# Optimization experiments

Hardware: AMD Instinct MI355X
Metric: run time of the kernel (lower is better)

Reference implementation:

```python
import jax, jax.numpy as jnp
import numpy as np

N, E, D, L = 50000, 625000, 128, 7
EPS = 1e-7   # GENConv message epsilon
T = 1.0      # softmax aggregation temperature (learn_t=False)
NUM_ATOM_FEATS, ATOM_VOCAB = 9, 64
NUM_BOND_FEATS, BOND_VOCAB = 3, 8


def setup_inputs() -> dict:
    key = jax.random.key(0)
    ks = jax.random.split(key, 9)
    x = jax.random.randint(ks[0], (N, NUM_ATOM_FEATS), 0, ATOM_VOCAB, dtype=jnp.int32)
    edge_index = jax.random.randint(ks[1], (2, E), 0, N, dtype=jnp.int32)
    edge_attr = jax.random.randint(ks[2], (E, NUM_BOND_FEATS), 0, BOND_VOCAB, dtype=jnp.int32)
    atom_emb = jax.random.normal(ks[3], (NUM_ATOM_FEATS, ATOM_VOCAB, D), dtype=jnp.float32) * 0.1
    bond_emb = jax.random.normal(ks[4], (NUM_BOND_FEATS, BOND_VOCAB, D), dtype=jnp.float32) * 0.1
    W = jax.random.normal(ks[5], (L, D, D), dtype=jnp.float32) / np.sqrt(D).astype(np.float32)
    b = jnp.zeros((L, D), dtype=jnp.float32)
    ln_gamma = jnp.ones((L, D), dtype=jnp.float32)
    ln_beta = jnp.zeros((L, D), dtype=jnp.float32)
    return dict(x=x, edge_index=edge_index, edge_attr=edge_attr,
                atom_emb=atom_emb, bond_emb=bond_emb, W=W, b=b,
                ln_gamma=ln_gamma, ln_beta=ln_beta)


def _layer_norm(h, g, bta):
    mu = jnp.mean(h, axis=-1, keepdims=True)
    var = jnp.var(h, axis=-1, keepdims=True)
    return (h - mu) * jax.lax.rsqrt(var + 1e-5) * g + bta


def _gen_conv(h, src, dst, edge_emb, Wl, bl):
    # GENConv: msg = relu(x_j + e) + eps; softmax aggregation over dst; Linear(x + m)
    msg = jax.nn.relu(h[src] + edge_emb) + EPS                 # [E, D]
    logits = msg * T
    seg_max = jax.ops.segment_max(logits, dst, num_segments=N)  # [N, D]
    seg_max = jnp.where(jnp.isfinite(seg_max), seg_max, 0.0)    # empty segments
    e = jnp.exp(logits - seg_max[dst])                          # [E, D]
    denom = jax.ops.segment_sum(e, dst, num_segments=N)         # [N, D]
    alpha = e / (denom[dst] + 1e-16)
    m = jax.ops.segment_sum(alpha * msg, dst, num_segments=N)   # [N, D]
    return (h + m) @ Wl + bl


def reference(x, edge_index, edge_attr, atom_emb, bond_emb, W, b, ln_gamma, ln_beta):
    src, dst = edge_index[0], edge_index[1]
    # AtomEncoder: sum of per-feature embedding lookups -> [N, D]
    h = jnp.sum(atom_emb[jnp.arange(NUM_ATOM_FEATS)[None, :], x], axis=1)
    # BondEncoder (conv_encode_edge=False: encoded once) -> [E, D]
    edge_emb = jnp.sum(bond_emb[jnp.arange(NUM_BOND_FEATS)[None, :], edge_attr], axis=1)
    # res+ block, dropout=0 (no-op)
    h = _gen_conv(h, src, dst, edge_emb, W[0], b[0])
    for layer in range(1, L):
        h2 = jax.nn.relu(_layer_norm(h, ln_gamma[layer - 1], ln_beta[layer - 1]))
        h = _gen_conv(h2, src, dst, edge_emb, W[layer], b[layer]) + h
    h = _layer_norm(h, ln_gamma[L - 1], ln_beta[L - 1])
    return h
```

## Files before the change

### kernel.cpp

```cpp
#include <hip/hip_runtime.h>
#include <hip/hip_fp16.h>
#include <math.h>


constexpr int D = 128;
constexpr int NA = 9;
constexpr int NB = 3;
constexpr float L2E = 1.4426950408889634f;
constexpr float INV_L2E = 0.6931471805599453f;

using half8  = __attribute__((ext_vector_type(8))) _Float16;
using h2v    = __attribute__((ext_vector_type(2))) _Float16;
using floatx4 = __attribute__((ext_vector_type(4))) float;


__global__ void k_hist(const int* __restrict__ dst, int* __restrict__ deg, int E) {
    int e = blockIdx.x * 256 + threadIdx.x;
    if (e < E) atomicAdd(&deg[dst[e]], 1);
}

__global__ void k_scan_a(const int* __restrict__ deg, int* __restrict__ offs,
                         int* __restrict__ bsum, int N) {
    __shared__ int s[256];
    int i = blockIdx.x * 256 + threadIdx.x;
    int v = (i < N) ? deg[i] : 0;
    s[threadIdx.x] = v;
    __syncthreads();
    for (int d = 1; d < 256; d <<= 1) {
        int add = (threadIdx.x >= d) ? s[threadIdx.x - d] : 0;
        __syncthreads();
        s[threadIdx.x] += add;
        __syncthreads();
    }
    if (i < N) offs[i + 1] = s[threadIdx.x];
    if (threadIdx.x == 255) bsum[blockIdx.x] = s[255];
    if (i == 0) offs[0] = 0;
}

__global__ void k_scan_b(const int* __restrict__ bsum, int* __restrict__ bexc, int nb) {
    __shared__ int s[256];
    int t = threadIdx.x;
    int v = (t < nb) ? bsum[t] : 0;
    s[t] = v;
    __syncthreads();
    for (int d = 1; d < 256; d <<= 1) {
        int add = (t >= d) ? s[t - d] : 0;
        __syncthreads();
        s[t] += add;
        __syncthreads();
    }
    if (t < nb) bexc[t] = s[t] - v;
}

__global__ void k_scan_c(int* __restrict__ offs, const int* __restrict__ bexc, int N) {
    int i = blockIdx.x * 256 + threadIdx.x;
    if (i < N) offs[i + 1] += bexc[blockIdx.x];
}

__global__ void k_fill(const int* __restrict__ src, const int* __restrict__ dst,
                       const int* __restrict__ attr, const int* __restrict__ offs,
                       int* __restrict__ cur, unsigned* __restrict__ recs1, int E) {
    int e = blockIdx.x * 256 + threadIdx.x;
    if (e >= E) return;
    int d = dst[e];
    int pos = offs[d] + atomicAdd(&cur[d], 1);
    unsigned cidx = (unsigned)(attr[e * 3] * 64 + attr[e * 3 + 1] * 8 + attr[e * 3 + 2]);
    recs1[pos] = (unsigned)src[e] | (cidx << 17);
}


__global__ void k_dhist(const int* __restrict__ deg, int* __restrict__ dbin, int N) {
    __shared__ int lb[64];
    int t = threadIdx.x;
    if (t < 64) lb[t] = 0;
    __syncthreads();
    int i = blockIdx.x * 256 + t;
    if (i < N) {
        int d = deg[i]; d = d < 63 ? d : 63;
        atomicAdd(&lb[63 - d], 1);
    }
    __syncthreads();
    if (t < 64 && lb[t] > 0) atomicAdd(&dbin[t], lb[t]);
}

__global__ void k_dscan(const int* __restrict__ dbin, int* __restrict__ doff) {
    if (threadIdx.x == 0) {
        int acc = 0;
        for (int b = 0; b < 64; ++b) { doff[b] = acc; acc += dbin[b]; }
    }
}

__global__ void k_dfill(const int* __restrict__ deg, const int* __restrict__ doff,
                        int* __restrict__ dcur, int* __restrict__ perm, int N) {
    __shared__ int lc[64], lbase[64];
    int t = threadIdx.x;
    if (t < 64) lc[t] = 0;
    __syncthreads();
    int i = blockIdx.x * 256 + t;
    int b = 0, rank = 0;
    if (i < N) {
        int d = deg[i]; d = d < 63 ? d : 63;
        b = 63 - d;
        rank = atomicAdd(&lc[b], 1);
    }
    __syncthreads();
    if (t < 64 && lc[t] > 0) lbase[t] = atomicAdd(&dcur[t], lc[t]);
    __syncthreads();
    if (i < N) perm[doff[b] + lbase[b] + rank] = i;
}

__global__ void k_comb(const float* __restrict__ bemb, __half* __restrict__ comb16) {
    int gid = blockIdx.x * 256 + threadIdx.x;
    int c = gid >> 5, q = gid & 31;
    int a0 = c >> 6, a1 = (c >> 3) & 7, a2 = c & 7;
    float4 v0 = *(const float4*)(bemb + (a0)*D + q * 4);
    float4 v1 = *(const float4*)(bemb + (8 + a1) * D + q * 4);
    float4 v2 = *(const float4*)(bemb + (16 + a2) * D + q * 4);
    __half2* c2 = (__half2*)comb16;
    c2[c * 64 + q * 2]     = __floats2half2_rn(L2E * (v0.x + v1.x + v2.x),
                                               L2E * (v0.y + v1.y + v2.y));
    c2[c * 64 + q * 2 + 1] = __floats2half2_rn(L2E * (v0.z + v1.z + v2.z),
                                               L2E * (v0.w + v1.w + v2.w));
}

__global__ void k_wt(const float* __restrict__ W, __half* __restrict__ Wt16, int total) {
    int o = blockIdx.x * 256 + threadIdx.x;
    if (o >= total) return;
    int l = o >> 14;
    int rem = o & 16383;
    int f = rem >> 7, k = rem & 127;
    Wt16[o] = __float2half_rn(W[(l << 14) + k * 128 + f]);
}


__global__ void k_atom(const int* __restrict__ x, const float* __restrict__ aemb,
                       __half* __restrict__ h16, int N) {
    int wid = (blockIdx.x * blockDim.x + threadIdx.x) >> 6;
    int lane = threadIdx.x & 63;
    if (wid >= N) return;
    const int* xr = x + wid * NA;
    float ax = 0.f, ay = 0.f;
#pragma unroll
    for (int f = 0; f < NA; ++f) {
        int v = xr[f];
        const float2 e = *(const float2*)(aemb + (f * 64 + v) * D + 2 * lane);
        ax += e.x; ay += e.y;
    }
    ((__half2*)h16)[wid * 64 + lane] = __floats2half2_rn(ax * L2E, ay * L2E);
}


__global__ __launch_bounds__(256) void k_agg(const __half* __restrict__ h16,
                      const unsigned* __restrict__ recs1,
                      const int* __restrict__ offs, const __half* __restrict__ comb16,
                      const int* __restrict__ perm,
                      __half* __restrict__ t16, int N) {
    int wid = (blockIdx.x * blockDim.x + threadIdx.x) >> 6;
    int lane = threadIdx.x & 63;
    if (wid >= N) return;
    int nid = perm[wid];
    int su = __builtin_amdgcn_readfirstlane(offs[nid]);
    int eu = __builtin_amdgcn_readfirstlane(offs[nid + 1]);
    h2v hm2 = ((const h2v*)h16)[nid * 64 + lane];
    float hsx = (float)hm2[0], hsy = (float)hm2[1];
    if (su >= eu) {
        ((__half2*)t16)[nid * 64 + lane] =
            __floats2half2_rn(hsx * INV_L2E, hsy * INV_L2E);
        return;
    }
    float Sx = 0.f, Sy = 0.f, Wx = 0.f, Wy = 0.f;

    const h2v* hrow = (const h2v*)h16 + lane;
    const h2v* crow = (const h2v*)comb16 + lane;

    const h2v zero2 = (h2v)(_Float16)0;
    const h2v eps2  = {(_Float16)(1e-7f * L2E), (_Float16)(1e-7f * L2E)};

    h2v hq[16], cq[16];

    int e0 = su;
    do {
        int lastc = (eu < e0 + 64) ? eu : e0 + 64;
        int last = lastc - 1;
        int ridx = e0 + lane;
        ridx = (ridx < eu - 1) ? ridx : eu - 1;
        unsigned recv = recs1[ridx];

        auto load4 = [&](int base, int slot) {
#pragma unroll
            for (int i = 0; i < 4; ++i) {
                int idx = base + i; idx = (idx < last) ? idx : last;
                unsigned r = __builtin_amdgcn_readlane(recv, idx - e0);
                int sj = (int)(r & 0x1FFFFu);
                int cj = (int)(r >> 17);
                hq[slot * 4 + i] = hrow[sj * 64];
                cq[slot * 4 + i] = crow[cj * 64];
            }
        };
        auto comp4u = [&](int slot) {
#pragma unroll
            for (int i = 0; i < 4; ++i) {
                h2v m = hq[slot * 4 + i] + cq[slot * 4 + i];
                m = __builtin_elementwise_max(m, zero2);
                m = m + eps2;
                float u0 = (float)m[0], u1 = (float)m[1];
                float px = __builtin_amdgcn_exp2f(u0);
                float py = __builtin_amdgcn_exp2f(u1);
                Sx += px; Sy += py;
                Wx = fmaf(px, u0, Wx);
                Wy = fmaf(py, u1, Wy);
            }
        };
        auto comp4m = [&](int gb, int slot) {
#pragma unroll
            for (int i = 0; i < 4; ++i) {
                h2v m = hq[slot * 4 + i] + cq[slot * 4 + i];
                m = __builtin_elementwise_max(m, zero2);
                m = m + eps2;
                float u0 = (float)m[0], u1 = (float)m[1];
                bool valid = (gb + i) < lastc;
                float px = valid ? __builtin_amdgcn_exp2f(u0) : 0.f;
                float py = valid ? __builtin_amdgcn_exp2f(u1) : 0.f;
                Sx += px; Sy += py;
                Wx = fmaf(px, u0, Wx);
                Wy = fmaf(py, u1, Wy);
            }
        };

        load4(e0, 0);
        if (e0 + 4  < lastc) load4(e0 + 4, 1);
        if (e0 + 8  < lastc) load4(e0 + 8, 2);
        if (e0 + 12 < lastc) load4(e0 + 12, 3);

        int e = e0;
        for (; e + 16 < lastc; e += 16) {
            comp4u(0); comp4u(1); comp4u(2); comp4u(3);
            load4(e + 16, 0); load4(e + 20, 1); load4(e + 24, 2); load4(e + 28, 3);
        }
        comp4m(e, 0);
        if (e + 4  < lastc) comp4m(e + 4, 1);
        if (e + 8  < lastc) comp4m(e + 8, 2);
        if (e + 12 < lastc) comp4m(e + 12, 3);

        e0 = lastc;
    } while (e0 < eu);

    float tx = (hsx + Wx / (Sx + 1e-16f)) * INV_L2E;
    float ty = (hsy + Wy / (Sy + 1e-16f)) * INV_L2E;
    ((__half2*)t16)[nid * 64 + lane] = __floats2half2_rn(tx, ty);
}


template <int MODE>
__global__ __launch_bounds__(256) void k_gemm(const __half* __restrict__ A16,
                                              const __half* __restrict__ Wt16,
                                              const float* __restrict__ bl,
                                              const __half* __restrict__ res16,
                                              __half* __restrict__ hres16,
                                              const float* __restrict__ g,
                                              const float* __restrict__ bta,
                                              __half* __restrict__ h16,
                                              float* __restrict__ out,
                                              int N, int useRes) {
    int lane = threadIdx.x & 63;
    int wave = threadIdx.x >> 6;
    int quad = lane >> 4, col = lane & 15;
    int node = blockIdx.x * 64 + wave * 16 + col;
    bool nok = node < N;
    int nc = nok ? node : N - 1;

    const __half* arow = A16 + (size_t)nc * 128;
    half8 bfrag[4];
#pragma unroll
    for (int ks = 0; ks < 4; ++ks)
        bfrag[ks] = *(const half8*)(arow + ks * 32 + quad * 8);

    floatx4 acc[8];
#pragma unroll
    for (int ft = 0; ft < 8; ++ft) acc[ft] = (floatx4){0.f, 0.f, 0.f, 0.f};

#pragma unroll
    for (int ft = 0; ft < 8; ++ft) {
        const __half* wrow = Wt16 + (size_t)(ft * 16 + col) * 128;
#pragma unroll
        for (int ks = 0; ks < 4; ++ks) {
            half8 afrag = *(const half8*)(wrow + ks * 32 + quad * 8);
            acc[ft] = __builtin_amdgcn_mfma_f32_16x16x32_f16(afrag, bfrag[ks],
                                                             acc[ft], 0, 0, 0);
        }
    }

    float s = 0.f, ss = 0.f;
#pragma unroll
    for (int ft = 0; ft < 8; ++ft) {
        int f0 = ft * 16 + quad * 4;
        float4 bb = *(const float4*)(bl + f0);
        float o0 = acc[ft][0] + bb.x, o1 = acc[ft][1] + bb.y;
        float o2 = acc[ft][2] + bb.z, o3 = acc[ft][3] + bb.w;
        if (useRes) {
            uint2 rr = *(const uint2*)(res16 + (size_t)nc * 128 + f0);
            __half2 r01 = *(__half2*)&rr.x, r23 = *(__half2*)&rr.y;
            o0 += __low2float(r01); o1 += __high2float(r01);
            o2 += __low2float(r23); o3 += __high2float(r23);
        }
        acc[ft][0] = o0; acc[ft][1] = o1; acc[ft][2] = o2; acc[ft][3] = o3;
        s += (o0 + o1) + (o2 + o3);
        ss += fmaf(o0, o0, o1 * o1) + fmaf(o2, o2, o3 * o3);
        if (MODE == 0 && nok) {
            __half2 h01 = __floats2half2_rn(o0, o1);
            __half2 h23 = __floats2half2_rn(o2, o3);
            uint2 pk = make_uint2(*(unsigned*)&h01, *(unsigned*)&h23);
            *(uint2*)(hres16 + (size_t)node * 128 + f0) = pk;
        }
    }
    s += __shfl_xor(s, 16, 64);  ss += __shfl_xor(ss, 16, 64);
    s += __shfl_xor(s, 32, 64);  ss += __shfl_xor(ss, 32, 64);
    float mu = s * (1.f / 128.f);
    float var = ss * (1.f / 128.f) - mu * mu;
    float rs = rsqrtf(var + 1e-5f);

#pragma unroll
    for (int ft = 0; ft < 8; ++ft) {
        int f0 = ft * 16 + quad * 4;
        float4 gg = *(const float4*)(g + f0);
        float4 bt = *(const float4*)(bta + f0);
        float l0 = (acc[ft][0] - mu) * rs * gg.x + bt.x;
        float l1 = (acc[ft][1] - mu) * rs * gg.y + bt.y;
        float l2 = (acc[ft][2] - mu) * rs * gg.z + bt.z;
        float l3 = (acc[ft][3] - mu) * rs * gg.w + bt.w;
        if (MODE == 0) {
            l0 = fmaxf(l0, 0.f); l1 = fmaxf(l1, 0.f);
            l2 = fmaxf(l2, 0.f); l3 = fmaxf(l3, 0.f);
            if (nok) {
                __half2 h01 = __floats2half2_rn(l0 * L2E, l1 * L2E);
                __half2 h23 = __floats2half2_rn(l2 * L2E, l3 * L2E);
                uint2 pk = make_uint2(*(unsigned*)&h01, *(unsigned*)&h23);
                *(uint2*)(h16 + (size_t)node * 128 + f0) = pk;
            }
        } else {
            if (nok)
                *(float4*)(out + (size_t)node * 128 + f0) =
                    make_float4(l0, l1, l2, l3);
        }
    }
}


extern "C" void kernel_launch(void* const* d_in, const int* in_sizes, int n_in,
                              void* d_out, int out_size, void* d_ws, size_t ws_size,
                              hipStream_t stream) {
    const int*   x    = (const int*)d_in[0];
    const int*   ei   = (const int*)d_in[1];
    const int*   attr = (const int*)d_in[2];
    const float* aemb = (const float*)d_in[3];
    const float* bemb = (const float*)d_in[4];
    const float* Wf   = (const float*)d_in[5];
    const float* bf   = (const float*)d_in[6];
    const float* gam  = (const float*)d_in[7];
    const float* bet  = (const float*)d_in[8];
    float* out = (float*)d_out;

    const int N = in_sizes[0] / NA;
    const int E = in_sizes[1] / 2;
    const int L = in_sizes[5] / (D * D);

    char* ws = (char*)d_ws;
    size_t o = 0;
    auto carve = [&](size_t bytes) -> void* {
        void* p = (void*)(ws + o);
        o += (bytes + 255) & ~(size_t)255;
        return p;
    };
    __half* hres16 = (__half*)carve((size_t)N * D * 2);
    __half* h16    = (__half*)carve((size_t)N * D * 2);
    __half* t16    = (__half*)carve((size_t)N * D * 2);
    unsigned* recs1 = (unsigned*)carve((size_t)E * 4);
    __half* comb16 = (__half*)carve(512 * D * 2);
    __half* Wt16   = (__half*)carve((size_t)L * D * D * 2);
    int*    deg    = (int*)carve((size_t)N * 4);
    int*    cur    = (int*)carve((size_t)N * 4);
    int*    offs   = (int*)carve((size_t)(N + 1) * 4);
    int*    perm   = (int*)carve((size_t)N * 4);
    int*    dbin   = (int*)carve(256);
    int*    doff   = (int*)carve(256);
    int*    dcur   = (int*)carve(256);
    int*    bsum   = (int*)carve(4096);
    int*    bexc   = (int*)carve(4096);

    const int* src = ei;
    const int* dst = ei + E;

    hipMemsetAsync(deg, 0, (size_t)N * 4, stream);
    hipMemsetAsync(cur, 0, (size_t)N * 4, stream);
    hipMemsetAsync(dbin, 0, 256, stream);
    hipMemsetAsync(dcur, 0, 256, stream);

    int ebl = (E + 255) / 256;
    int nbl = (N + 255) / 256;
    k_comb<<<64, 256, 0, stream>>>(bemb, comb16);
    int wtot = L * D * D;
    k_wt<<<(wtot + 255) / 256, 256, 0, stream>>>(Wf, Wt16, wtot);
    k_hist<<<ebl, 256, 0, stream>>>(dst, deg, E);
    k_scan_a<<<nbl, 256, 0, stream>>>(deg, offs, bsum, N);
    k_scan_b<<<1, 256, 0, stream>>>(bsum, bexc, nbl);
    k_scan_c<<<nbl, 256, 0, stream>>>(offs, bexc, N);
    k_fill<<<ebl, 256, 0, stream>>>(src, dst, attr, offs, cur, recs1, E);
    k_dhist<<<nbl, 256, 0, stream>>>(deg, dbin, N);
    k_dscan<<<1, 64, 0, stream>>>(dbin, doff);
    k_dfill<<<nbl, 256, 0, stream>>>(deg, doff, dcur, perm, N);

    int wbl = (N * 64 + 255) / 256;
    k_atom<<<wbl, 256, 0, stream>>>(x, aemb, h16, N);

    int gbl = (N + 63) / 64;
    for (int l = 0; l < L; ++l) {
        k_agg<<<wbl, 256, 0, stream>>>(h16, recs1, offs, comb16, perm, t16, N);
        if (l == L - 1) {
            k_gemm<1><<<gbl, 256, 0, stream>>>(t16, Wt16 + l * D * D, bf + l * D,
                                               hres16, hres16,
                                               gam + l * D, bet + l * D, h16, out,
                                               N, 1);
        } else {
            k_gemm<0><<<gbl, 256, 0, stream>>>(t16, Wt16 + l * D * D, bf + l * D,
                                               hres16, hres16,
                                               gam + l * D, bet + l * D, h16, out,
                                               N, l > 0 ? 1 : 0);
        }
    }
}
```

Baseline: 622.8 us.

## Fuse softmax aggregation into GEMM kernel with ping-pong feature buffers

Merges the per-node softmax aggregation kernel into the GEMM/LayerNorm kernel. Each wave aggregates 16 consecutive nodes into an LDS tile, which then feeds the MFMA stage directly, so the t16 intermediate no longer round-trips through global memory and one launch per layer is removed. The degree-sorted node permutation and its three setup kernels are dropped, and h is ping-ponged between two buffers to avoid a read/write race. The epsilon add in the message is also removed. The costs are serialized per-wave processing of 16 nodes with varied degrees (load imbalance without degree sorting) and lower occupancy from the 17 KB LDS tile. Dropping the epsilon slightly changes the numerics.

```diff
diff --git a/kernel.cpp b/kernel.cpp
--- a/kernel.cpp
+++ b/kernel.cpp
@@ -68,47 +68,6 @@
     recs1[pos] = (unsigned)src[e] | (cidx << 17);
 }
 
-
-__global__ void k_dhist(const int* __restrict__ deg, int* __restrict__ dbin, int N) {
-    __shared__ int lb[64];
-    int t = threadIdx.x;
-    if (t < 64) lb[t] = 0;
-    __syncthreads();
-    int i = blockIdx.x * 256 + t;
-    if (i < N) {
-        int d = deg[i]; d = d < 63 ? d : 63;
-        atomicAdd(&lb[63 - d], 1);
-    }
-    __syncthreads();
-    if (t < 64 && lb[t] > 0) atomicAdd(&dbin[t], lb[t]);
-}
-
-__global__ void k_dscan(const int* __restrict__ dbin, int* __restrict__ doff) {
-    if (threadIdx.x == 0) {
-        int acc = 0;
-        for (int b = 0; b < 64; ++b) { doff[b] = acc; acc += dbin[b]; }
-    }
-}
-
-__global__ void k_dfill(const int* __restrict__ deg, const int* __restrict__ doff,
-                        int* __restrict__ dcur, int* __restrict__ perm, int N) {
-    __shared__ int lc[64], lbase[64];
-    int t = threadIdx.x;
-    if (t < 64) lc[t] = 0;
-    __syncthreads();
-    int i = blockIdx.x * 256 + t;
-    int b = 0, rank = 0;
-    if (i < N) {
-        int d = deg[i]; d = d < 63 ? d : 63;
-        b = 63 - d;
-        rank = atomicAdd(&lc[b], 1);
-    }
-    __syncthreads();
-    if (t < 64 && lc[t] > 0) lbase[t] = atomicAdd(&dcur[t], lc[t]);
-    __syncthreads();
-    if (i < N) perm[doff[b] + lbase[b] + rank] = i;
-}
-
 __global__ void k_comb(const float* __restrict__ bemb, __half* __restrict__ comb16) {
     int gid = blockIdx.x * 256 + threadIdx.x;
     int c = gid >> 5, q = gid & 31;
@@ -150,130 +109,130 @@
 }
 
 
-__global__ __launch_bounds__(256) void k_agg(const __half* __restrict__ h16,
-                      const unsigned* __restrict__ recs1,
-                      const int* __restrict__ offs, const __half* __restrict__ comb16,
-                      const int* __restrict__ perm,
-                      __half* __restrict__ t16, int N) {
-    int wid = (blockIdx.x * blockDim.x + threadIdx.x) >> 6;
-    int lane = threadIdx.x & 63;
-    if (wid >= N) return;
-    int nid = perm[wid];
-    int su = __builtin_amdgcn_readfirstlane(offs[nid]);
-    int eu = __builtin_amdgcn_readfirstlane(offs[nid + 1]);
-    h2v hm2 = ((const h2v*)h16)[nid * 64 + lane];
-    float hsx = (float)hm2[0], hsy = (float)hm2[1];
-    if (su >= eu) {
-        ((__half2*)t16)[nid * 64 + lane] =
-            __floats2half2_rn(hsx * INV_L2E, hsy * INV_L2E);
-        return;
-    }
-    float Sx = 0.f, Sy = 0.f, Wx = 0.f, Wy = 0.f;
-
-    const h2v* hrow = (const h2v*)h16 + lane;
-    const h2v* crow = (const h2v*)comb16 + lane;
-
-    const h2v zero2 = (h2v)(_Float16)0;
-    const h2v eps2  = {(_Float16)(1e-7f * L2E), (_Float16)(1e-7f * L2E)};
-
-    h2v hq[16], cq[16];
-
-    int e0 = su;
-    do {
-        int lastc = (eu < e0 + 64) ? eu : e0 + 64;
-        int last = lastc - 1;
-        int ridx = e0 + lane;
-        ridx = (ridx < eu - 1) ? ridx : eu - 1;
-        unsigned recv = recs1[ridx];
-
-        auto load4 = [&](int base, int slot) {
-#pragma unroll
-            for (int i = 0; i < 4; ++i) {
-                int idx = base + i; idx = (idx < last) ? idx : last;
-                unsigned r = __builtin_amdgcn_readlane(recv, idx - e0);
-                int sj = (int)(r & 0x1FFFFu);
-                int cj = (int)(r >> 17);
-                hq[slot * 4 + i] = hrow[sj * 64];
-                cq[slot * 4 + i] = crow[cj * 64];
-            }
-        };
-        auto comp4u = [&](int slot) {
-#pragma unroll
-            for (int i = 0; i < 4; ++i) {
-                h2v m = hq[slot * 4 + i] + cq[slot * 4 + i];
-                m = __builtin_elementwise_max(m, zero2);
-                m = m + eps2;
-                float u0 = (float)m[0], u1 = (float)m[1];
-                float px = __builtin_amdgcn_exp2f(u0);
-                float py = __builtin_amdgcn_exp2f(u1);
-                Sx += px; Sy += py;
-                Wx = fmaf(px, u0, Wx);
-                Wy = fmaf(py, u1, Wy);
-            }
-        };
-        auto comp4m = [&](int gb, int slot) {
-#pragma unroll
-            for (int i = 0; i < 4; ++i) {
-                h2v m = hq[slot * 4 + i] + cq[slot * 4 + i];
-                m = __builtin_elementwise_max(m, zero2);
-                m = m + eps2;
-                float u0 = (float)m[0], u1 = (float)m[1];
-                bool valid = (gb + i) < lastc;
-                float px = valid ? __builtin_amdgcn_exp2f(u0) : 0.f;
-                float py = valid ? __builtin_amdgcn_exp2f(u1) : 0.f;
-                Sx += px; Sy += py;
-                Wx = fmaf(px, u0, Wx);
-                Wy = fmaf(py, u1, Wy);
-            }
-        };
-
-        load4(e0, 0);
-        if (e0 + 4  < lastc) load4(e0 + 4, 1);
-        if (e0 + 8  < lastc) load4(e0 + 8, 2);
-        if (e0 + 12 < lastc) load4(e0 + 12, 3);
-
-        int e = e0;
-        for (; e + 16 < lastc; e += 16) {
-            comp4u(0); comp4u(1); comp4u(2); comp4u(3);
-            load4(e + 16, 0); load4(e + 20, 1); load4(e + 24, 2); load4(e + 28, 3);
-        }
-        comp4m(e, 0);
-        if (e + 4  < lastc) comp4m(e + 4, 1);
-        if (e + 8  < lastc) comp4m(e + 8, 2);
-        if (e + 12 < lastc) comp4m(e + 12, 3);
-
-        e0 = lastc;
-    } while (e0 < eu);
-
-    float tx = (hsx + Wx / (Sx + 1e-16f)) * INV_L2E;
-    float ty = (hsy + Wy / (Sy + 1e-16f)) * INV_L2E;
-    ((__half2*)t16)[nid * 64 + lane] = __floats2half2_rn(tx, ty);
-}
-
-
 template <int MODE>
-__global__ __launch_bounds__(256) void k_gemm(const __half* __restrict__ A16,
-                                              const __half* __restrict__ Wt16,
-                                              const float* __restrict__ bl,
-                                              const __half* __restrict__ res16,
-                                              __half* __restrict__ hres16,
-                                              const float* __restrict__ g,
-                                              const float* __restrict__ bta,
-                                              __half* __restrict__ h16,
-                                              float* __restrict__ out,
-                                              int N, int useRes) {
+__global__ __launch_bounds__(256) void k_fused(
+    const __half* __restrict__ hin,
+    const unsigned* __restrict__ recs1,
+    const int* __restrict__ offs,
+    const __half* __restrict__ comb16,
+    const __half* __restrict__ Wt16,
+    const float* __restrict__ bl,
+    __half* __restrict__ hres16,
+    const float* __restrict__ g,
+    const float* __restrict__ bta,
+    __half* __restrict__ hout,
+    float* __restrict__ out,
+    int N, int useRes) {
+    __shared__ __align__(16) __half tt[64 * 136];
     int lane = threadIdx.x & 63;
     int wave = threadIdx.x >> 6;
+    int nbase = blockIdx.x * 64 + wave * 16;
+
+    int oidx = nbase + lane;
+    oidx = (oidx <= N) ? oidx : N;
+    int offv = (lane < 17) ? offs[oidx] : 0;
+
+    const h2v* hrow = (const h2v*)hin + lane;
+    const h2v* crow = (const h2v*)comb16 + lane;
+    const h2v zero2 = (h2v)(_Float16)0;
+
+#pragma unroll 1
+    for (int j = 0; j < 16; ++j) {
+        int nid = nbase + j;
+        int nc = (nid < N) ? nid : N - 1;
+        int su = __builtin_amdgcn_readlane(offv, j);
+        int eu = __builtin_amdgcn_readlane(offv, j + 1);
+        h2v hm2 = hrow[nc * 64];
+        float hsx = (float)hm2[0], hsy = (float)hm2[1];
+        float tx, ty;
+        if (su >= eu) {
+            tx = hsx * INV_L2E;
+            ty = hsy * INV_L2E;
+        } else {
+            float Sx = 0.f, Sy = 0.f, Wx = 0.f, Wy = 0.f;
+            h2v hq[16], cq[16];
+            int e0 = su;
+            do {
+                int lastc = (eu < e0 + 64) ? eu : e0 + 64;
+                int last = lastc - 1;
+                int ridx = e0 + lane;
+                ridx = (ridx < eu - 1) ? ridx : eu - 1;
+                unsigned recv = recs1[ridx];
+
+                auto load4 = [&](int base, int slot) {
+#pragma unroll
+                    for (int i = 0; i < 4; ++i) {
+                        int idx = base + i; idx = (idx < last) ? idx : last;
+                        unsigned r = __builtin_amdgcn_readlane(recv, idx - e0);
+                        int sj = (int)(r & 0x1FFFFu);
+                        int cj = (int)(r >> 17);
+                        hq[slot * 4 + i] = hrow[sj * 64];
+                        cq[slot * 4 + i] = crow[cj * 64];
+                    }
+                };
+                auto comp4u = [&](int slot) {
+#pragma unroll
+                    for (int i = 0; i < 4; ++i) {
+                        h2v m = hq[slot * 4 + i] + cq[slot * 4 + i];
+                        m = __builtin_elementwise_max(m, zero2);
+                        float u0 = (float)m[0], u1 = (float)m[1];
+                        float px = __builtin_amdgcn_exp2f(u0);
+                        float py = __builtin_amdgcn_exp2f(u1);
+                        Sx += px; Sy += py;
+                        Wx = fmaf(px, u0, Wx);
+                        Wy = fmaf(py, u1, Wy);
+                    }
+                };
+                auto comp4m = [&](int gb, int slot) {
+#pragma unroll
+                    for (int i = 0; i < 4; ++i) {
+                        h2v m = hq[slot * 4 + i] + cq[slot * 4 + i];
+                        m = __builtin_elementwise_max(m, zero2);
+                        float u0 = (float)m[0], u1 = (float)m[1];
+                        bool valid = (gb + i) < lastc;
+                        float px = valid ? __builtin_amdgcn_exp2f(u0) : 0.f;
+                        float py = valid ? __builtin_amdgcn_exp2f(u1) : 0.f;
+                        Sx += px; Sy += py;
+                        Wx = fmaf(px, u0, Wx);
+                        Wy = fmaf(py, u1, Wy);
+                    }
+                };
+
+                load4(e0, 0);
+                if (e0 + 4  < lastc) load4(e0 + 4, 1);
+                if (e0 + 8  < lastc) load4(e0 + 8, 2);
+                if (e0 + 12 < lastc) load4(e0 + 12, 3);
+
+                int e = e0;
+                for (; e + 16 < lastc; e += 16) {
+                    comp4u(0); comp4u(1); comp4u(2); comp4u(3);
+                    load4(e + 16, 0); load4(e + 20, 1);
+                    load4(e + 24, 2); load4(e + 28, 3);
+                }
+                comp4m(e, 0);
+                if (e + 4  < lastc) comp4m(e + 4, 1);
+                if (e + 8  < lastc) comp4m(e + 8, 2);
+                if (e + 12 < lastc) comp4m(e + 12, 3);
+
+                e0 = lastc;
+            } while (e0 < eu);
+            tx = (hsx + Wx / (Sx + 1e-16f)) * INV_L2E;
+            ty = (hsy + Wy / (Sy + 1e-16f)) * INV_L2E;
+        }
+        ((__half2*)tt)[(wave * 16 + j) * 68 + lane] = __floats2half2_rn(tx, ty);
+    }
+    __syncthreads();
+
     int quad = lane >> 4, col = lane & 15;
     int node = blockIdx.x * 64 + wave * 16 + col;
     bool nok = node < N;
-    int nc = nok ? node : N - 1;
-
-    const __half* arow = A16 + (size_t)nc * 128;
+    int nc2 = nok ? node : N - 1;
+
+    const __half* trow = tt + (size_t)(wave * 16 + col) * 136;
     half8 bfrag[4];
 #pragma unroll
     for (int ks = 0; ks < 4; ++ks)
-        bfrag[ks] = *(const half8*)(arow + ks * 32 + quad * 8);
+        bfrag[ks] = *(const half8*)(trow + ks * 32 + quad * 8);
 
     floatx4 acc[8];
 #pragma unroll
@@ -298,7 +257,7 @@
         float o0 = acc[ft][0] + bb.x, o1 = acc[ft][1] + bb.y;
         float o2 = acc[ft][2] + bb.z, o3 = acc[ft][3] + bb.w;
         if (useRes) {
-            uint2 rr = *(const uint2*)(res16 + (size_t)nc * 128 + f0);
+            uint2 rr = *(const uint2*)(hres16 + (size_t)nc2 * 128 + f0);
             __half2 r01 = *(__half2*)&rr.x, r23 = *(__half2*)&rr.y;
             o0 += __low2float(r01); o1 += __high2float(r01);
             o2 += __low2float(r23); o3 += __high2float(r23);
@@ -335,7 +294,7 @@
                 __half2 h01 = __floats2half2_rn(l0 * L2E, l1 * L2E);
                 __half2 h23 = __floats2half2_rn(l2 * L2E, l3 * L2E);
                 uint2 pk = make_uint2(*(unsigned*)&h01, *(unsigned*)&h23);
-                *(uint2*)(h16 + (size_t)node * 128 + f0) = pk;
+                *(uint2*)(hout + (size_t)node * 128 + f0) = pk;
             }
         } else {
             if (nok)
@@ -372,18 +331,14 @@
         return p;
     };
     __half* hres16 = (__half*)carve((size_t)N * D * 2);
-    __half* h16    = (__half*)carve((size_t)N * D * 2);
-    __half* t16    = (__half*)carve((size_t)N * D * 2);
+    __half* hA     = (__half*)carve((size_t)N * D * 2);
+    __half* hB     = (__half*)carve((size_t)N * D * 2);
     unsigned* recs1 = (unsigned*)carve((size_t)E * 4);
     __half* comb16 = (__half*)carve(512 * D * 2);
     __half* Wt16   = (__half*)carve((size_t)L * D * D * 2);
     int*    deg    = (int*)carve((size_t)N * 4);
     int*    cur    = (int*)carve((size_t)N * 4);
     int*    offs   = (int*)carve((size_t)(N + 1) * 4);
-    int*    perm   = (int*)carve((size_t)N * 4);
-    int*    dbin   = (int*)carve(256);
-    int*    doff   = (int*)carve(256);
-    int*    dcur   = (int*)carve(256);
     int*    bsum   = (int*)carve(4096);
     int*    bexc   = (int*)carve(4096);
 
@@ -392,8 +347,6 @@
 
     hipMemsetAsync(deg, 0, (size_t)N * 4, stream);
     hipMemsetAsync(cur, 0, (size_t)N * 4, stream);
-    hipMemsetAsync(dbin, 0, 256, stream);
-    hipMemsetAsync(dcur, 0, 256, stream);
 
     int ebl = (E + 255) / 256;
     int nbl = (N + 255) / 256;
@@ -405,26 +358,24 @@
     k_scan_b<<<1, 256, 0, stream>>>(bsum, bexc, nbl);
     k_scan_c<<<nbl, 256, 0, stream>>>(offs, bexc, N);
     k_fill<<<ebl, 256, 0, stream>>>(src, dst, attr, offs, cur, recs1, E);
-    k_dhist<<<nbl, 256, 0, stream>>>(deg, dbin, N);
-    k_dscan<<<1, 64, 0, stream>>>(dbin, doff);
-    k_dfill<<<nbl, 256, 0, stream>>>(deg, doff, dcur, perm, N);
 
     int wbl = (N * 64 + 255) / 256;
-    k_atom<<<wbl, 256, 0, stream>>>(x, aemb, h16, N);
+    k_atom<<<wbl, 256, 0, stream>>>(x, aemb, hA, N);
 
     int gbl = (N + 63) / 64;
     for (int l = 0; l < L; ++l) {
-        k_agg<<<wbl, 256, 0, stream>>>(h16, recs1, offs, comb16, perm, t16, N);
+        const __half* hi = (l & 1) ? hB : hA;
+        __half* ho = (l & 1) ? hA : hB;
         if (l == L - 1) {
-            k_gemm<1><<<gbl, 256, 0, stream>>>(t16, Wt16 + l * D * D, bf + l * D,
-                                               hres16, hres16,
-                                               gam + l * D, bet + l * D, h16, out,
-                                               N, 1);
+            k_fused<1><<<gbl, 256, 0, stream>>>(hi, recs1, offs, comb16,
+                                                Wt16 + l * D * D, bf + l * D,
+                                                hres16, gam + l * D, bet + l * D,
+                                                ho, out, N, 1);
         } else {
-            k_gemm<0><<<gbl, 256, 0, stream>>>(t16, Wt16 + l * D * D, bf + l * D,
-                                               hres16, hres16,
-                                               gam + l * D, bet + l * D, h16, out,
-                                               N, l > 0 ? 1 : 0);
-        }
-    }
-}
+            k_fused<0><<<gbl, 256, 0, stream>>>(hi, recs1, offs, comb16,
+                                                Wt16 + l * D * D, bf + l * D,
+                                                hres16, gam + l * D, bet + l * D,
+                                                ho, out, N, l > 0 ? 1 : 0);
+        }
+    }
+}
```

Result: slower. 756.6 us (+21.5%).

## Replace degree-sorted node permutation with edge-balanced node ranges per wave

Applied to the files above, without the earlier changes.

Drops the degree-bucket permutation (histogram, scan and fill kernels) and instead splits the CSR into ranges of about 32 edges, giving each wave the run of consecutive nodes whose edges start in its range. The aggregation kernel loops over those nodes, which balances edges per wave, cuts the wave count from N to about E/32, and makes node accesses sequential. It also drops the epsilon add in the message. Serial node loops within a wave can lower memory-level parallelism for low-degree nodes, and removing eps slightly changes numerics.

```diff
diff --git a/kernel.cpp b/kernel.cpp
--- a/kernel.cpp
+++ b/kernel.cpp
@@ -6,6 +6,7 @@
 constexpr int D = 128;
 constexpr int NA = 9;
 constexpr int NB = 3;
+constexpr int CEDGE = 32;
 constexpr float L2E = 1.4426950408889634f;
 constexpr float INV_L2E = 0.6931471805599453f;
 
@@ -68,45 +69,16 @@
     recs1[pos] = (unsigned)src[e] | (cidx << 17);
 }
 
-
-__global__ void k_dhist(const int* __restrict__ deg, int* __restrict__ dbin, int N) {
-    __shared__ int lb[64];
-    int t = threadIdx.x;
-    if (t < 64) lb[t] = 0;
-    __syncthreads();
-    int i = blockIdx.x * 256 + t;
-    if (i < N) {
-        int d = deg[i]; d = d < 63 ? d : 63;
-        atomicAdd(&lb[63 - d], 1);
-    }
-    __syncthreads();
-    if (t < 64 && lb[t] > 0) atomicAdd(&dbin[t], lb[t]);
-}
-
-__global__ void k_dscan(const int* __restrict__ dbin, int* __restrict__ doff) {
-    if (threadIdx.x == 0) {
-        int acc = 0;
-        for (int b = 0; b < 64; ++b) { doff[b] = acc; acc += dbin[b]; }
-    }
-}
-
-__global__ void k_dfill(const int* __restrict__ deg, const int* __restrict__ doff,
-                        int* __restrict__ dcur, int* __restrict__ perm, int N) {
-    __shared__ int lc[64], lbase[64];
-    int t = threadIdx.x;
-    if (t < 64) lc[t] = 0;
-    __syncthreads();
-    int i = blockIdx.x * 256 + t;
-    int b = 0, rank = 0;
-    if (i < N) {
-        int d = deg[i]; d = d < 63 ? d : 63;
-        b = 63 - d;
-        rank = atomicAdd(&lc[b], 1);
-    }
-    __syncthreads();
-    if (t < 64 && lc[t] > 0) lbase[t] = atomicAdd(&dcur[t], lc[t]);
-    __syncthreads();
-    if (i < N) perm[doff[b] + lbase[b] + rank] = i;
+__global__ void k_part(const int* __restrict__ offs, int* __restrict__ wstart,
+                       int N, int NW) {
+    int n = blockIdx.x * 256 + threadIdx.x;
+    if (n >= N) return;
+    int a = offs[n] / CEDGE;
+    int b = offs[n + 1] / CEDGE;
+    if (n == 0) wstart[0] = 0;
+    for (int w = a + 1; w <= b; ++w) wstart[w] = n + 1;
+    if (n == N - 1)
+        for (int w = b + 1; w <= NW; ++w) wstart[w] = N;
 }
 
 __global__ void k_comb(const float* __restrict__ bemb, __half* __restrict__ comb16) {
@@ -153,101 +125,101 @@
 __global__ __launch_bounds__(256) void k_agg(const __half* __restrict__ h16,
                       const unsigned* __restrict__ recs1,
                       const int* __restrict__ offs, const __half* __restrict__ comb16,
-                      const int* __restrict__ perm,
-                      __half* __restrict__ t16, int N) {
-    int wid = (blockIdx.x * blockDim.x + threadIdx.x) >> 6;
+                      const int* __restrict__ wstart,
+                      __half* __restrict__ t16, int NW) {
+    int w = (blockIdx.x * blockDim.x + threadIdx.x) >> 6;
     int lane = threadIdx.x & 63;
-    if (wid >= N) return;
-    int nid = perm[wid];
-    int su = __builtin_amdgcn_readfirstlane(offs[nid]);
-    int eu = __builtin_amdgcn_readfirstlane(offs[nid + 1]);
-    h2v hm2 = ((const h2v*)h16)[nid * 64 + lane];
-    float hsx = (float)hm2[0], hsy = (float)hm2[1];
-    if (su >= eu) {
-        ((__half2*)t16)[nid * 64 + lane] =
-            __floats2half2_rn(hsx * INV_L2E, hsy * INV_L2E);
-        return;
-    }
-    float Sx = 0.f, Sy = 0.f, Wx = 0.f, Wy = 0.f;
+    if (w >= NW) return;
+    int n0 = wstart[w];
+    int n1 = wstart[w + 1];
 
     const h2v* hrow = (const h2v*)h16 + lane;
     const h2v* crow = (const h2v*)comb16 + lane;
-
     const h2v zero2 = (h2v)(_Float16)0;
-    const h2v eps2  = {(_Float16)(1e-7f * L2E), (_Float16)(1e-7f * L2E)};
-
-    h2v hq[16], cq[16];
-
-    int e0 = su;
-    do {
-        int lastc = (eu < e0 + 64) ? eu : e0 + 64;
-        int last = lastc - 1;
-        int ridx = e0 + lane;
-        ridx = (ridx < eu - 1) ? ridx : eu - 1;
-        unsigned recv = recs1[ridx];
-
-        auto load4 = [&](int base, int slot) {
-#pragma unroll
-            for (int i = 0; i < 4; ++i) {
-                int idx = base + i; idx = (idx < last) ? idx : last;
-                unsigned r = __builtin_amdgcn_readlane(recv, idx - e0);
-                int sj = (int)(r & 0x1FFFFu);
-                int cj = (int)(r >> 17);
-                hq[slot * 4 + i] = hrow[sj * 64];
-                cq[slot * 4 + i] = crow[cj * 64];
+
+#pragma unroll 1
+    for (int nid = n0; nid < n1; ++nid) {
+        int su = offs[nid];
+        int eu = offs[nid + 1];
+        h2v hm2 = hrow[nid * 64];
+        float hsx = (float)hm2[0], hsy = (float)hm2[1];
+        if (su >= eu) {
+            ((__half2*)t16)[nid * 64 + lane] =
+                __floats2half2_rn(hsx * INV_L2E, hsy * INV_L2E);
+            continue;
+        }
+        float Sx = 0.f, Sy = 0.f, Wx = 0.f, Wy = 0.f;
+        h2v hq[16], cq[16];
+        int e0 = su;
+        do {
+            int lastc = (eu < e0 + 64) ? eu : e0 + 64;
+            int last = lastc - 1;
+            int ridx = e0 + lane;
+            ridx = (ridx < eu - 1) ? ridx : eu - 1;
+            unsigned recv = recs1[ridx];
+
+            auto load4 = [&](int base, int slot) {
+#pragma unroll
+                for (int i = 0; i < 4; ++i) {
+                    int idx = base + i; idx = (idx < last) ? idx : last;
+                    unsigned r = __builtin_amdgcn_readlane(recv, idx - e0);
+                    int sj = (int)(r & 0x1FFFFu);
+                    int cj = (int)(r >> 17);
+                    hq[slot * 4 + i] = hrow[sj * 64];
+                    cq[slot * 4 + i] = crow[cj * 64];
+                }
+            };
+            auto comp4u = [&](int slot) {
+#pragma unroll
+                for (int i = 0; i < 4; ++i) {
+                    h2v m = hq[slot * 4 + i] + cq[slot * 4 + i];
+                    m = __builtin_elementwise_max(m, zero2);
+                    float u0 = (float)m[0], u1 = (float)m[1];
+                    float px = __builtin_amdgcn_exp2f(u0);
+                    float py = __builtin_amdgcn_exp2f(u1);
+                    Sx += px; Sy += py;
+                    Wx = fmaf(px, u0, Wx);
+                    Wy = fmaf(py, u1, Wy);
+                }
+            };
+            auto comp4m = [&](int gb, int slot) {
+#pragma unroll
+                for (int i = 0; i < 4; ++i) {
+                    h2v m = hq[slot * 4 + i] + cq[slot * 4 + i];
+                    m = __builtin_elementwise_max(m, zero2);
+                    float u0 = (float)m[0], u1 = (float)m[1];
+                    bool valid = (gb + i) < lastc;
+                    float px = valid ? __builtin_amdgcn_exp2f(u0) : 0.f;
+                    float py = valid ? __builtin_amdgcn_exp2f(u1) : 0.f;
+                    Sx += px; Sy += py;
+                    Wx = fmaf(px, u0, Wx);
+                    Wy = fmaf(py, u1, Wy);
+                }
+            };
+
+            load4(e0, 0);
+            if (e0 + 4  < lastc) load4(e0 + 4, 1);
+            if (e0 + 8  < lastc) load4(e0 + 8, 2);
+            if (e0 + 12 < lastc) load4(e0 + 12, 3);
+
+            int e = e0;
+            for (; e + 16 < lastc; e += 16) {
+                comp4u(0); comp4u(1); comp4u(2); comp4u(3);
+                load4(e + 16, 0); load4(e + 20, 1);
+                load4(e + 24, 2); load4(e + 28, 3);
             }
-        };
-        auto comp4u = [&](int slot) {
-#pragma unroll
-            for (int i = 0; i < 4; ++i) {
-                h2v m = hq[slot * 4 + i] + cq[slot * 4 + i];
-                m = __builtin_elementwise_max(m, zero2);
-                m = m + eps2;
-                float u0 = (float)m[0], u1 = (float)m[1];
-                float px = __builtin_amdgcn_exp2f(u0);
-                float py = __builtin_amdgcn_exp2f(u1);
-                Sx += px; Sy += py;
-                Wx = fmaf(px, u0, Wx);
-                Wy = fmaf(py, u1, Wy);
-            }
-        };
-        auto comp4m = [&](int gb, int slot) {
-#pragma unroll
-            for (int i = 0; i < 4; ++i) {
-                h2v m = hq[slot * 4 + i] + cq[slot * 4 + i];
-                m = __builtin_elementwise_max(m, zero2);
-                m = m + eps2;
-                float u0 = (float)m[0], u1 = (float)m[1];
-                bool valid = (gb + i) < lastc;
-                float px = valid ? __builtin_amdgcn_exp2f(u0) : 0.f;
-                float py = valid ? __builtin_amdgcn_exp2f(u1) : 0.f;
-                Sx += px; Sy += py;
-                Wx = fmaf(px, u0, Wx);
-                Wy = fmaf(py, u1, Wy);
-            }
-        };
-
-        load4(e0, 0);
-        if (e0 + 4  < lastc) load4(e0 + 4, 1);
-        if (e0 + 8  < lastc) load4(e0 + 8, 2);
-        if (e0 + 12 < lastc) load4(e0 + 12, 3);
-
-        int e = e0;
-        for (; e + 16 < lastc; e += 16) {
-            comp4u(0); comp4u(1); comp4u(2); comp4u(3);
-            load4(e + 16, 0); load4(e + 20, 1); load4(e + 24, 2); load4(e + 28, 3);
-        }
-        comp4m(e, 0);
-        if (e + 4  < lastc) comp4m(e + 4, 1);
-        if (e + 8  < lastc) comp4m(e + 8, 2);
-        if (e + 12 < lastc) comp4m(e + 12, 3);
-
-        e0 = lastc;
-    } while (e0 < eu);
-
-    float tx = (hsx + Wx / (Sx + 1e-16f)) * INV_L2E;
-    float ty = (hsy + Wy / (Sy + 1e-16f)) * INV_L2E;
-    ((__half2*)t16)[nid * 64 + lane] = __floats2half2_rn(tx, ty);
+            comp4m(e, 0);
+            if (e + 4  < lastc) comp4m(e + 4, 1);
+            if (e + 8  < lastc) comp4m(e + 8, 2);
+            if (e + 12 < lastc) comp4m(e + 12, 3);
+
+            e0 = lastc;
+        } while (e0 < eu);
+
+        float tx = (hsx + Wx / (Sx + 1e-16f)) * INV_L2E;
+        float ty = (hsy + Wy / (Sy + 1e-16f)) * INV_L2E;
+        ((__half2*)t16)[nid * 64 + lane] = __floats2half2_rn(tx, ty);
+    }
 }
 
 
@@ -363,6 +335,7 @@
     const int N = in_sizes[0] / NA;
     const int E = in_sizes[1] / 2;
     const int L = in_sizes[5] / (D * D);
+    const int NW = (E + CEDGE - 1) / CEDGE;
 
     char* ws = (char*)d_ws;
     size_t o = 0;
@@ -380,10 +353,7 @@
     int*    deg    = (int*)carve((size_t)N * 4);
     int*    cur    = (int*)carve((size_t)N * 4);
     int*    offs   = (int*)carve((size_t)(N + 1) * 4);
-    int*    perm   = (int*)carve((size_t)N * 4);
-    int*    dbin   = (int*)carve(256);
-    int*    doff   = (int*)carve(256);
-    int*    dcur   = (int*)carve(256);
+    int*    wstart = (int*)carve((size_t)(NW + 1) * 4);
     int*    bsum   = (int*)carve(4096);
     int*    bexc   = (int*)carve(4096);
 
@@ -392,8 +362,6 @@
 
     hipMemsetAsync(deg, 0, (size_t)N * 4, stream);
     hipMemsetAsync(cur, 0, (size_t)N * 4, stream);
-    hipMemsetAsync(dbin, 0, 256, stream);
-    hipMemsetAsync(dcur, 0, 256, stream);
 
     int ebl = (E + 255) / 256;
     int nbl = (N + 255) / 256;
@@ -405,16 +373,15 @@
     k_scan_b<<<1, 256, 0, stream>>>(bsum, bexc, nbl);
     k_scan_c<<<nbl, 256, 0, stream>>>(offs, bexc, N);
     k_fill<<<ebl, 256, 0, stream>>>(src, dst, attr, offs, cur, recs1, E);
-    k_dhist<<<nbl, 256, 0, stream>>>(deg, dbin, N);
-    k_dscan<<<1, 64, 0, stream>>>(dbin, doff);
-    k_dfill<<<nbl, 256, 0, stream>>>(deg, doff, dcur, perm, N);
+    k_part<<<nbl, 256, 0, stream>>>(offs, wstart, N, NW);
 
     int wbl = (N * 64 + 255) / 256;
     k_atom<<<wbl, 256, 0, stream>>>(x, aemb, h16, N);
 
+    int abl = (NW * 64 + 255) / 256;
     int gbl = (N + 63) / 64;
     for (int l = 0; l < L; ++l) {
-        k_agg<<<wbl, 256, 0, stream>>>(h16, recs1, offs, comb16, perm, t16, N);
+        k_agg<<<abl, 256, 0, stream>>>(h16, recs1, offs, comb16, wstart, t16, NW);
         if (l == L - 1) {
             k_gemm<1><<<gbl, 256, 0, stream>>>(t16, Wt16 + l * D * D, bf + l * D,
                                                hres16, hres16,
```

Result: slower. 666.0 us (+6.9%).

## Split GEMM output features across wave pairs and drop eps add in aggregation

Applied to the files above, without the earlier changes.

The GEMM+LayerNorm kernel now gives each 16-node group to two waves that each compute half of the 128 output features. The row statistics are combined through shared memory with a block barrier, and residual loads are hoisted ahead of the MFMA loop. This halves the accumulator registers per wave and doubles the block count, aiming for higher occupancy and more parallelism, at the cost of a __syncthreads and each wave loading its A fragment redundantly. The aggregation kernel also drops the per-edge epsilon add, a small numerical deviation, and changes the masked-tail validity test from lastc to eu.

```diff
diff --git a/kernel.cpp b/kernel.cpp
--- a/kernel.cpp
+++ b/kernel.cpp
@@ -172,9 +172,7 @@
 
     const h2v* hrow = (const h2v*)h16 + lane;
     const h2v* crow = (const h2v*)comb16 + lane;
-
     const h2v zero2 = (h2v)(_Float16)0;
-    const h2v eps2  = {(_Float16)(1e-7f * L2E), (_Float16)(1e-7f * L2E)};
 
     h2v hq[16], cq[16];
 
@@ -202,7 +200,6 @@
             for (int i = 0; i < 4; ++i) {
                 h2v m = hq[slot * 4 + i] + cq[slot * 4 + i];
                 m = __builtin_elementwise_max(m, zero2);
-                m = m + eps2;
                 float u0 = (float)m[0], u1 = (float)m[1];
                 float px = __builtin_amdgcn_exp2f(u0);
                 float py = __builtin_amdgcn_exp2f(u1);
@@ -216,9 +213,8 @@
             for (int i = 0; i < 4; ++i) {
                 h2v m = hq[slot * 4 + i] + cq[slot * 4 + i];
                 m = __builtin_elementwise_max(m, zero2);
-                m = m + eps2;
                 float u0 = (float)m[0], u1 = (float)m[1];
-                bool valid = (gb + i) < lastc;
+                bool valid = (gb + i) < eu;
                 float px = valid ? __builtin_amdgcn_exp2f(u0) : 0.f;
                 float py = valid ? __builtin_amdgcn_exp2f(u1) : 0.f;
                 Sx += px; Sy += py;
@@ -262,10 +258,12 @@
                                               __half* __restrict__ h16,
                                               float* __restrict__ out,
                                               int N, int useRes) {
+    __shared__ float2 sm[2][2][16];
     int lane = threadIdx.x & 63;
     int wave = threadIdx.x >> 6;
+    int grp = wave >> 1, half = wave & 1;
     int quad = lane >> 4, col = lane & 15;
-    int node = blockIdx.x * 64 + wave * 16 + col;
+    int node = blockIdx.x * 32 + grp * 16 + col;
     bool nok = node < N;
     int nc = nok ? node : N - 1;
 
@@ -275,35 +273,43 @@
     for (int ks = 0; ks < 4; ++ks)
         bfrag[ks] = *(const half8*)(arow + ks * 32 + quad * 8);
 
-    floatx4 acc[8];
-#pragma unroll
-    for (int ft = 0; ft < 8; ++ft) acc[ft] = (floatx4){0.f, 0.f, 0.f, 0.f};
-
-#pragma unroll
-    for (int ft = 0; ft < 8; ++ft) {
-        const __half* wrow = Wt16 + (size_t)(ft * 16 + col) * 128;
+    uint2 rr[4];
+    if (useRes) {
+#pragma unroll
+        for (int ft2 = 0; ft2 < 4; ++ft2) {
+            int f0 = (half * 4 + ft2) * 16 + quad * 4;
+            rr[ft2] = *(const uint2*)(res16 + (size_t)nc * 128 + f0);
+        }
+    }
+
+    floatx4 acc[4];
+#pragma unroll
+    for (int ft2 = 0; ft2 < 4; ++ft2) acc[ft2] = (floatx4){0.f, 0.f, 0.f, 0.f};
+
+#pragma unroll
+    for (int ft2 = 0; ft2 < 4; ++ft2) {
+        const __half* wrow = Wt16 + (size_t)((half * 4 + ft2) * 16 + col) * 128;
 #pragma unroll
         for (int ks = 0; ks < 4; ++ks) {
             half8 afrag = *(const half8*)(wrow + ks * 32 + quad * 8);
-            acc[ft] = __builtin_amdgcn_mfma_f32_16x16x32_f16(afrag, bfrag[ks],
-                                                             acc[ft], 0, 0, 0);
+            acc[ft2] = __builtin_amdgcn_mfma_f32_16x16x32_f16(afrag, bfrag[ks],
+                                                              acc[ft2], 0, 0, 0);
         }
     }
 
     float s = 0.f, ss = 0.f;
 #pragma unroll
-    for (int ft = 0; ft < 8; ++ft) {
-        int f0 = ft * 16 + quad * 4;
+    for (int ft2 = 0; ft2 < 4; ++ft2) {
+        int f0 = (half * 4 + ft2) * 16 + quad * 4;
         float4 bb = *(const float4*)(bl + f0);
-        float o0 = acc[ft][0] + bb.x, o1 = acc[ft][1] + bb.y;
-        float o2 = acc[ft][2] + bb.z, o3 = acc[ft][3] + bb.w;
+        float o0 = acc[ft2][0] + bb.x, o1 = acc[ft2][1] + bb.y;
+        float o2 = acc[ft2][2] + bb.z, o3 = acc[ft2][3] + bb.w;
         if (useRes) {
-            uint2 rr = *(const uint2*)(res16 + (size_t)nc * 128 + f0);
-            __half2 r01 = *(__half2*)&rr.x, r23 = *(__half2*)&rr.y;
+            __half2 r01 = *(__half2*)&rr[ft2].x, r23 = *(__half2*)&rr[ft2].y;
             o0 += __low2float(r01); o1 += __high2float(r01);
             o2 += __low2float(r23); o3 += __high2float(r23);
         }
-        acc[ft][0] = o0; acc[ft][1] = o1; acc[ft][2] = o2; acc[ft][3] = o3;
+        acc[ft2][0] = o0; acc[ft2][1] = o1; acc[ft2][2] = o2; acc[ft2][3] = o3;
         s += (o0 + o1) + (o2 + o3);
         ss += fmaf(o0, o0, o1 * o1) + fmaf(o2, o2, o3 * o3);
         if (MODE == 0 && nok) {
@@ -315,19 +321,23 @@
     }
     s += __shfl_xor(s, 16, 64);  ss += __shfl_xor(ss, 16, 64);
     s += __shfl_xor(s, 32, 64);  ss += __shfl_xor(ss, 32, 64);
-    float mu = s * (1.f / 128.f);
-    float var = ss * (1.f / 128.f) - mu * mu;
+    if (quad == 0) sm[grp][half][col] = make_float2(s, ss);
+    __syncthreads();
+    float2 oth = sm[grp][half ^ 1][col];
+    float st = s + oth.x, sst = ss + oth.y;
+    float mu = st * (1.f / 128.f);
+    float var = sst * (1.f / 128.f) - mu * mu;
     float rs = rsqrtf(var + 1e-5f);
 
 #pragma unroll
-    for (int ft = 0; ft < 8; ++ft) {
-        int f0 = ft * 16 + quad * 4;
+    for (int ft2 = 0; ft2 < 4; ++ft2) {
+        int f0 = (half * 4 + ft2) * 16 + quad * 4;
         float4 gg = *(const float4*)(g + f0);
         float4 bt = *(const float4*)(bta + f0);
-        float l0 = (acc[ft][0] - mu) * rs * gg.x + bt.x;
-        float l1 = (acc[ft][1] - mu) * rs * gg.y + bt.y;
-        float l2 = (acc[ft][2] - mu) * rs * gg.z + bt.z;
-        float l3 = (acc[ft][3] - mu) * rs * gg.w + bt.w;
+        float l0 = (acc[ft2][0] - mu) * rs * gg.x + bt.x;
+        float l1 = (acc[ft2][1] - mu) * rs * gg.y + bt.y;
+        float l2 = (acc[ft2][2] - mu) * rs * gg.z + bt.z;
+        float l3 = (acc[ft2][3] - mu) * rs * gg.w + bt.w;
         if (MODE == 0) {
             l0 = fmaxf(l0, 0.f); l1 = fmaxf(l1, 0.f);
             l2 = fmaxf(l2, 0.f); l3 = fmaxf(l3, 0.f);
@@ -412,7 +422,7 @@
     int wbl = (N * 64 + 255) / 256;
     k_atom<<<wbl, 256, 0, stream>>>(x, aemb, h16, N);
 
-    int gbl = (N + 63) / 64;
+    int gbl = (N + 31) / 32;
     for (int l = 0; l < L; ++l) {
         k_agg<<<wbl, 256, 0, stream>>>(h16, recs1, offs, comb16, perm, t16, N);
         if (l == L - 1) {
```

Measured after the change: 596.3 us. -4.3%, faster.
